# Optimization experiments

Measured on AMD Instinct MI355X. Metric: run time of the kernel, lower is better.

The kernel has to match this reference:

```python
import jax, jax.numpy as jnp
import numpy as np

N = 100000
H = 512
NUM_HEADS = 8
G = 512  # number of graphs (segments)


def seg_softmax(s, batch, num_segments):
    # numerically stable segment softmax (PyG-style, +1e-16 in denom)
    m = jax.ops.segment_max(s, batch, num_segments=num_segments)
    e = jnp.exp(s - m[batch])
    d = jax.ops.segment_sum(e, batch, num_segments=num_segments)
    return e / (d[batch] + 1e-16)


def setup_inputs() -> dict:
    key = jax.random.key(0)
    ks = jax.random.split(key, 12)
    s = 0.02
    x = jax.random.normal(ks[0], (N, H), dtype=jnp.float32)
    batch = jnp.sort(jax.random.randint(ks[1], (N,), 0, G)).astype(jnp.int64)
    # GlobalAttention.gate_nn: Linear(H, H//2) -> ReLU -> Linear(H//2, 1)
    ga_g_w1 = jax.random.normal(ks[2], (H, H // 2), dtype=jnp.float32) * s
    ga_g_b1 = jnp.zeros((H // 2,), dtype=jnp.float32)
    ga_g_w2 = jax.random.normal(ks[3], (H // 2, 1), dtype=jnp.float32) * s
    ga_g_b2 = jnp.zeros((1,), dtype=jnp.float32)
    # GlobalAttention.nn: Linear(H, H) -> ReLU
    ga_n_w = jax.random.normal(ks[4], (H, H), dtype=jnp.float32) * s
    ga_n_b = jnp.zeros((H,), dtype=jnp.float32)
    # outer gate_nn: Linear(H, H) -> ReLU -> (Dropout: identity in eval) -> Linear(H, NUM_HEADS)
    g_w1 = jax.random.normal(ks[5], (H, H), dtype=jnp.float32) * s
    g_b1 = jnp.zeros((H,), dtype=jnp.float32)
    g_w2 = jax.random.normal(ks[6], (H, NUM_HEADS), dtype=jnp.float32) * s
    g_b2 = jnp.zeros((NUM_HEADS,), dtype=jnp.float32)
    return dict(x=x, batch=batch,
                ga_g_w1=ga_g_w1, ga_g_b1=ga_g_b1, ga_g_w2=ga_g_w2, ga_g_b2=ga_g_b2,
                ga_n_w=ga_n_w, ga_n_b=ga_n_b,
                g_w1=g_w1, g_b1=g_b1, g_w2=g_w2, g_b2=g_b2)


def reference(x, batch, ga_g_w1, ga_g_b1, ga_g_w2, ga_g_b2, ga_n_w, ga_n_b,
              g_w1, g_b1, g_w2, g_b2):
    # --- GlobalAttention pooling ---
    h = jax.nn.relu(x @ ga_g_w1 + ga_g_b1)          # (N, H//2)
    gate = (h @ ga_g_w2 + ga_g_b2)[:, 0]            # (N,)
    gate = seg_softmax(gate, batch, G)              # segment softmax per graph
    xt = jax.nn.relu(x @ ga_n_w + ga_n_b)           # (N, H)
    graph_embedding = jax.ops.segment_sum(gate[:, None] * xt, batch,
                                          num_segments=G)  # (G, H)
    # --- interpretable attention weights ---
    g = jax.nn.relu(x @ g_w1 + g_b1)                # (N, H); dropout = identity (eval)
    scores = (g @ g_w2 + g_b2).mean(axis=-1)        # (N,) mean over heads
    attention = seg_softmax(scores, batch, G)       # (N,)
    return graph_embedding, attention
```

## Files before the change

kernel.cpp:

```cpp
#include <hip/hip_runtime.h>

#define NN 100000
#define HH 512
#define GG 512
#define NPACK 1280
#define NSTRIP 40
#define SB 32768
#define SB16 16384
#define XTROWS (NN + 128)

typedef unsigned short u16;
typedef unsigned int u32;
typedef __bf16 bf16x8 __attribute__((ext_vector_type(8)));
typedef unsigned short u16x8 __attribute__((ext_vector_type(8)));
typedef float f32x4 __attribute__((ext_vector_type(4)));
typedef __attribute__((address_space(1))) void gvoid_t;
typedef __attribute__((address_space(3))) void lvoid_t;

__device__ __forceinline__ u16 f2bf(float f) {
    unsigned u = __float_as_uint(f);
    unsigned r = u + 0x7FFFu + ((u >> 16) & 1u);
    return (u16)(r >> 16);
}
__device__ __forceinline__ float bf2f(u16 b) {
    return __uint_as_float(((unsigned)b) << 16);
}

__global__ __launch_bounds__(256)
void k_prep(const float* __restrict__ gw1, const float* __restrict__ gb1,
            const float* __restrict__ gw2v,
            const float* __restrict__ nw, const float* __restrict__ nbias,
            const float* __restrict__ aw1, const float* __restrict__ ab1,
            const float* __restrict__ aw2, const int* __restrict__ batch,
            u16* __restrict__ WT, float2* __restrict__ bwv,
            int* __restrict__ starts) {
    __shared__ u16 lt[64][80];
    const int b = blockIdx.x, tid = threadIdx.x;
    if (b < 160) {
        const int bn = b >> 3, bk = b & 7;
        const int N0 = bn * 64, K0 = bk * 64;
        const float* src; int LD, nb0;
        if (N0 < 256)      { src = gw1; LD = 256; nb0 = N0; }
        else if (N0 < 768) { src = nw;  LD = 512; nb0 = N0 - 256; }
        else               { src = aw1; LD = 512; nb0 = N0 - 768; }
        const int kr = tid >> 2, q = tid & 3;
        const float* sp = src + (size_t)(K0 + kr) * LD + nb0 + q * 16;
#pragma unroll
        for (int jj = 0; jj < 4; ++jj) {
            float4 f = *(const float4*)(sp + jj * 4);
            lt[q * 16 + jj * 4 + 0][kr] = f2bf(f.x);
            lt[q * 16 + jj * 4 + 1][kr] = f2bf(f.y);
            lt[q * 16 + jj * 4 + 2][kr] = f2bf(f.z);
            lt[q * 16 + jj * 4 + 3][kr] = f2bf(f.w);
        }
        __syncthreads();
        const int nlcl = tid >> 2, c2 = tid & 3;
        const int n = N0 + nlcl;
        const int s = n >> 4, nl = n & 15;
#pragma unroll
        for (int cc = 0; cc < 2; ++cc) {
            int c = c2 * 2 + cc;
            int ckb = (K0 >> 3) + c;
            size_t byte = (size_t)s * SB16 + nl * 1024 + ((size_t)(ckb ^ nl) << 4);
            *(u16x8*)((char*)WT + byte) = *(const u16x8*)(&lt[nlcl][c * 8]);
        }
    } else {
        for (int n = tid; n < NPACK; n += 256) {
            float bi, wv;
            if (n < 256)      { bi = gb1[n];        wv = gw2v[n]; }
            else if (n < 768) { bi = nbias[n - 256]; wv = 0.f; }
            else {
                bi = ab1[n - 768];
                float s = 0.f;
                for (int h = 0; h < 8; ++h) s += aw2[(n - 768) * 8 + h];
                wv = s * 0.125f;
            }
            bwv[n] = make_float2(bi, wv);
        }
        for (int g = tid; g <= GG; g += 256) {
            if (g == GG) { starts[GG] = NN; continue; }
            int lo = 0, hi = NN;
            while (lo < hi) { int mid = (lo + hi) >> 1; if (batch[mid] < g) lo = mid + 1; else hi = mid; }
            starts[g] = lo;
        }
    }
}

__global__ __launch_bounds__(256, 2)
void k_gemm(const float* __restrict__ X, const u16* __restrict__ B,
            const float2* __restrict__ bwv,
            const float* __restrict__ gb2, const float* __restrict__ ab2,
            u16* __restrict__ xt, float* __restrict__ gs, float* __restrict__ as_) {
    __shared__ __align__(16) char ldsB[2 * SB];
    __shared__ __align__(8) float2 bwv_lds[NPACK];

    const int tid = threadIdx.x;
    const int lane = tid & 63;
    const int w = tid >> 6;
    const int m0 = blockIdx.x * 128;
    const int l16 = lane & 15, kq = lane >> 4;

#define STAGE(s, bsel) do {                                                          \
    const char* _src = (const char*)B + (size_t)(s) * SB + tid * 16;                 \
    char* _dst = ldsB + (bsel) * SB + tid * 16;                                      \
    _Pragma("unroll")                                                                \
    for (int _t = 0; _t < 8; ++_t)                                                   \
        __builtin_amdgcn_global_load_lds((gvoid_t*)(_src + _t * 4096),               \
                                         (lvoid_t*)(_dst + _t * 4096), 16, 0, 0);    \
} while (0)

    STAGE(0, 0);

    for (int t = tid; t < NPACK; t += 256) bwv_lds[t] = bwv[t];

    float b2 = gb2[0];
    float bb = 0.f;
#pragma unroll
    for (int h = 0; h < 8; ++h) bb += ab2[h];
    bb *= 0.125f;

    bf16x8 a_reg[2][16];
#pragma unroll
    for (int i = 0; i < 2; ++i) {
        int row = m0 + w * 32 + i * 16 + l16;
        if (row >= NN) row = NN - 1;
        const float* xp = X + (size_t)row * 512 + kq * 8;
#pragma unroll
        for (int kt = 0; kt < 16; ++kt) {
            float4 f0 = *(const float4*)(xp + kt * 32);
            float4 f1 = *(const float4*)(xp + kt * 32 + 4);
            u16x8 u;
            u[0] = f2bf(f0.x); u[1] = f2bf(f0.y); u[2] = f2bf(f0.z); u[3] = f2bf(f0.w);
            u[4] = f2bf(f1.x); u[5] = f2bf(f1.y); u[6] = f2bf(f1.z); u[7] = f2bf(f1.w);
            a_reg[i][kt] = __builtin_bit_cast(bf16x8, u);
        }
    }

    float s_[2][4];
#pragma unroll
    for (int i = 0; i < 2; ++i)
#pragma unroll
        for (int r = 0; r < 4; ++r) s_[i][r] = 0.f;

    __syncthreads();

    for (int nt = 0; nt < NSTRIP; ++nt) {
        const int cur = nt & 1;

        if (nt >= 8 && nt <= 24) asm volatile("s_waitcnt vmcnt(8)" ::: "memory");
        else                     asm volatile("s_waitcnt vmcnt(0)" ::: "memory");
        __builtin_amdgcn_s_barrier();
        __builtin_amdgcn_sched_barrier(0);

        if (nt + 1 < NSTRIP) STAGE(nt + 1, cur ^ 1);

        f32x4 acc[2][2];
#pragma unroll
        for (int i = 0; i < 2; ++i) { acc[i][0] = {0.f,0.f,0.f,0.f}; acc[i][1] = {0.f,0.f,0.f,0.f}; }

        const char* bbase = ldsB + cur * SB + l16 * 1024;
        __builtin_amdgcn_s_setprio(1);
#pragma unroll
        for (int kt = 0; kt < 16; ++kt) {
            int off = ((kt * 4 + kq) ^ l16) << 4;
            bf16x8 b0 = *(const bf16x8*)(bbase + off);
            bf16x8 b1 = *(const bf16x8*)(bbase + 16384 + off);
#pragma unroll
            for (int i = 0; i < 2; ++i) {
                acc[i][0] = __builtin_amdgcn_mfma_f32_16x16x32_bf16(a_reg[i][kt], b0, acc[i][0], 0, 0, 0);
                acc[i][1] = __builtin_amdgcn_mfma_f32_16x16x32_bf16(a_reg[i][kt], b1, acc[i][1], 0, 0, 0);
            }
        }
        __builtin_amdgcn_s_setprio(0);

        float2 bw0 = bwv_lds[nt * 32 + l16];
        float2 bw1 = bwv_lds[nt * 32 + 16 + l16];
        if (nt >= 8 && nt < 24) {
            const int sx = nt - 8;
#pragma unroll
            for (int i = 0; i < 2; ++i)
#pragma unroll
                for (int r = 0; r < 4; ++r) {
                    int rg = m0 + w * 32 + i * 16 + kq * 4 + r;
                    ushort2 st;
                    st.x = f2bf(fmaxf(acc[i][0][r] + bw0.x, 0.f));
                    st.y = f2bf(fmaxf(acc[i][1][r] + bw1.x, 0.f));
                    *(ushort2*)(xt + (size_t)rg * 512 + sx * 32 + l16 * 2) = st;
                }
        } else {
#pragma unroll
            for (int i = 0; i < 2; ++i)
#pragma unroll
                for (int r = 0; r < 4; ++r)
                    s_[i][r] += fmaxf(acc[i][0][r] + bw0.x, 0.f) * bw0.y
                              + fmaxf(acc[i][1][r] + bw1.x, 0.f) * bw1.y;
            if (nt == 7) {
#pragma unroll
                for (int i = 0; i < 2; ++i)
#pragma unroll
                    for (int r = 0; r < 4; ++r) {
                        float pg = s_[i][r];
                        pg += __shfl_xor(pg, 1); pg += __shfl_xor(pg, 2);
                        pg += __shfl_xor(pg, 4); pg += __shfl_xor(pg, 8);
                        int rg = m0 + w * 32 + i * 16 + kq * 4 + r;
                        if (l16 == 0 && rg < NN) gs[rg] = pg + b2;
                        s_[i][r] = 0.f;
                    }
            }
        }
    }
#undef STAGE

#pragma unroll
    for (int i = 0; i < 2; ++i)
#pragma unroll
        for (int r = 0; r < 4; ++r) {
            float pa = s_[i][r];
            pa += __shfl_xor(pa, 1); pa += __shfl_xor(pa, 2);
            pa += __shfl_xor(pa, 4); pa += __shfl_xor(pa, 8);
            int rg = m0 + w * 32 + i * 16 + kq * 4 + r;
            if (l16 == 0 && rg < NN) as_[rg] = pa + bb;
        }
}

__global__ __launch_bounds__(256)
void k_post(const float* __restrict__ gs, const float* __restrict__ as_,
            const u16* __restrict__ xt, const int* __restrict__ starts,
            float* __restrict__ out_emb, float* __restrict__ out_att) {
    const int g = blockIdx.x;
    const int s0 = starts[g], s1 = starts[g + 1];
    const int tid = threadIdx.x, lane = tid & 63, w = tid >> 6;
    __shared__ float red[8];
    __shared__ float gbuf[1024];

    float lmg = -3.0e38f, lma = -3.0e38f;
    for (int i = s0 + tid; i < s1; i += 256) {
        lmg = fmaxf(lmg, gs[i]); lma = fmaxf(lma, as_[i]);
    }
    for (int o = 32; o; o >>= 1) {
        lmg = fmaxf(lmg, __shfl_xor(lmg, o));
        lma = fmaxf(lma, __shfl_xor(lma, o));
    }
    if (lane == 0) { red[w] = lmg; red[4 + w] = lma; }
    __syncthreads();
    float Mg = fmaxf(fmaxf(red[0], red[1]), fmaxf(red[2], red[3]));
    float Ma = fmaxf(fmaxf(red[4], red[5]), fmaxf(red[6], red[7]));
    __syncthreads();
    float sgv = 0.f, sav = 0.f;
    for (int i = s0 + tid; i < s1; i += 256) {
        sgv += expf(gs[i] - Mg); sav += expf(as_[i] - Ma);
    }
    for (int o = 32; o; o >>= 1) { sgv += __shfl_xor(sgv, o); sav += __shfl_xor(sav, o); }
    if (lane == 0) { red[w] = sgv; red[4 + w] = sav; }
    __syncthreads();
    const float Dg = red[0] + red[1] + red[2] + red[3] + 1e-16f;
    const float Da = red[4] + red[5] + red[6] + red[7] + 1e-16f;

    const int c2 = tid;
    const int col0 = (c2 >> 4) * 32 + (c2 & 15);
    float a0 = 0.f, a1 = 0.f;
    for (int nb = s0; nb < s1; nb += 1024) {
        const int ce = min(s1, nb + 1024);
        __syncthreads();
        for (int i = nb + tid; i < ce; i += 256) {
            gbuf[i - nb] = expf(gs[i] - Mg) / Dg;
            out_att[i]   = expf(as_[i] - Ma) / Da;
        }
        __syncthreads();
        const int cl = ce - nb;
        int j = 0;
        for (; j + 4 <= cl; j += 4) {
            const size_t n = (size_t)(nb + j);
            ushort2 u0 = ((const ushort2*)(xt + (n + 0) * 512))[c2];
            ushort2 u1 = ((const ushort2*)(xt + (n + 1) * 512))[c2];
            ushort2 u2 = ((const ushort2*)(xt + (n + 2) * 512))[c2];
            ushort2 u3 = ((const ushort2*)(xt + (n + 3) * 512))[c2];
            float g0 = gbuf[j], g1 = gbuf[j + 1], g2 = gbuf[j + 2], g3 = gbuf[j + 3];
            a0 += g0 * bf2f(u0.x); a1 += g0 * bf2f(u0.y);
            a0 += g1 * bf2f(u1.x); a1 += g1 * bf2f(u1.y);
            a0 += g2 * bf2f(u2.x); a1 += g2 * bf2f(u2.y);
            a0 += g3 * bf2f(u3.x); a1 += g3 * bf2f(u3.y);
        }
        for (; j < cl; ++j) {
            ushort2 u = ((const ushort2*)(xt + (size_t)(nb + j) * 512))[c2];
            float gj = gbuf[j];
            a0 += gj * bf2f(u.x); a1 += gj * bf2f(u.y);
        }
    }
    out_emb[g * 512 + col0] = a0;
    out_emb[g * 512 + col0 + 16] = a1;
}

extern "C" void kernel_launch(void* const* d_in, const int* in_sizes, int n_in,
                              void* d_out, int out_size, void* d_ws, size_t ws_size,
                              hipStream_t stream) {
    const float* x       = (const float*)d_in[0];
    const int*   batch   = (const int*)d_in[1];
    const float* ga_g_w1 = (const float*)d_in[2];
    const float* ga_g_b1 = (const float*)d_in[3];
    const float* ga_g_w2 = (const float*)d_in[4];
    const float* ga_g_b2 = (const float*)d_in[5];
    const float* ga_n_w  = (const float*)d_in[6];
    const float* ga_n_b  = (const float*)d_in[7];
    const float* g_w1    = (const float*)d_in[8];
    const float* g_b1    = (const float*)d_in[9];
    const float* g_w2    = (const float*)d_in[10];
    const float* g_b2    = (const float*)d_in[11];

    float* out_emb = (float*)d_out;
    float* out_att = out_emb + GG * HH;

    char* p = (char*)d_ws;
    size_t off = 0;
    auto alloc = [&](size_t bytes) -> char* {
        char* q = p + off;
        off += (bytes + 255) & ~(size_t)255;
        return q;
    };
    u16*    xt    = (u16*)   alloc((size_t)XTROWS * HH * 2);
    u16*    WT    = (u16*)   alloc((size_t)NPACK * 512 * 2);
    float2* bwv   = (float2*)alloc(NPACK * 8);
    float*  gs    = (float*) alloc((size_t)NN * 4);
    float*  as_   = (float*) alloc((size_t)NN * 4);
    int*    starts= (int*)   alloc((GG + 1) * 4);

    k_prep<<<161, 256, 0, stream>>>(ga_g_w1, ga_g_b1, ga_g_w2, ga_n_w, ga_n_b,
                                    g_w1, g_b1, g_w2, batch, WT, bwv, starts);
    k_gemm<<<782, 256, 0, stream>>>(x, WT, bwv, ga_g_b2, g_b2, xt, gs, as_);
    k_post<<<GG, 256, 0, stream>>>(gs, as_, xt, starts, out_emb, out_att);
}
```

Before: 487.0 us.

## Read packed weights directly from global memory instead of LDS double-buffering

The GEMM kernel stops staging weight strips into LDS through async global-to-LDS loads with double buffering and barriers. Each wave now loads its B fragments straight from a plain row-major packed weight layout in global memory, relying on L1/L2 caching, and reads the bias/weight pairs from global memory too. The prep kernel writes that unswizzled layout. The post kernel's segment-sum loop is also unrolled from 4 to 8 rows. This removes LDS traffic and barriers and frees LDS for occupancy, but the four waves now issue redundant global loads and lose explicit prefetch overlap.

```diff
diff --git a/kernel.cpp b/kernel.cpp
--- a/kernel.cpp
+++ b/kernel.cpp
@@ -5,8 +5,6 @@
 #define GG 512
 #define NPACK 1280
 #define NSTRIP 40
-#define SB 32768
-#define SB16 16384
 #define XTROWS (NN + 128)
 
 typedef unsigned short u16;
@@ -14,8 +12,6 @@
 typedef __bf16 bf16x8 __attribute__((ext_vector_type(8)));
 typedef unsigned short u16x8 __attribute__((ext_vector_type(8)));
 typedef float f32x4 __attribute__((ext_vector_type(4)));
-typedef __attribute__((address_space(1))) void gvoid_t;
-typedef __attribute__((address_space(3))) void lvoid_t;
 
 __device__ __forceinline__ u16 f2bf(float f) {
     unsigned u = __float_as_uint(f);
@@ -56,12 +52,10 @@
         __syncthreads();
         const int nlcl = tid >> 2, c2 = tid & 3;
         const int n = N0 + nlcl;
-        const int s = n >> 4, nl = n & 15;
 #pragma unroll
         for (int cc = 0; cc < 2; ++cc) {
             int c = c2 * 2 + cc;
-            int ckb = (K0 >> 3) + c;
-            size_t byte = (size_t)s * SB16 + nl * 1024 + ((size_t)(ckb ^ nl) << 4);
+            size_t byte = (size_t)n * 1024 + (size_t)(K0 / 8 + c) * 16;
             *(u16x8*)((char*)WT + byte) = *(const u16x8*)(&lt[nlcl][c * 8]);
         }
     } else {
@@ -91,27 +85,11 @@
             const float2* __restrict__ bwv,
             const float* __restrict__ gb2, const float* __restrict__ ab2,
             u16* __restrict__ xt, float* __restrict__ gs, float* __restrict__ as_) {
-    __shared__ __align__(16) char ldsB[2 * SB];
-    __shared__ __align__(8) float2 bwv_lds[NPACK];
-
     const int tid = threadIdx.x;
     const int lane = tid & 63;
     const int w = tid >> 6;
     const int m0 = blockIdx.x * 128;
     const int l16 = lane & 15, kq = lane >> 4;
-
-#define STAGE(s, bsel) do {                                                          \
-    const char* _src = (const char*)B + (size_t)(s) * SB + tid * 16;                 \
-    char* _dst = ldsB + (bsel) * SB + tid * 16;                                      \
-    _Pragma("unroll")                                                                \
-    for (int _t = 0; _t < 8; ++_t)                                                   \
-        __builtin_amdgcn_global_load_lds((gvoid_t*)(_src + _t * 4096),               \
-                                         (lvoid_t*)(_dst + _t * 4096), 16, 0, 0);    \
-} while (0)
-
-    STAGE(0, 0);
-
-    for (int t = tid; t < NPACK; t += 256) bwv_lds[t] = bwv[t];
 
     float b2 = gb2[0];
     float bb = 0.f;
@@ -142,39 +120,29 @@
 #pragma unroll
         for (int r = 0; r < 4; ++r) s_[i][r] = 0.f;
 
-    __syncthreads();
+    const u16* bp = B + (size_t)l16 * 512 + kq * 8;
 
     for (int nt = 0; nt < NSTRIP; ++nt) {
-        const int cur = nt & 1;
-
-        if (nt >= 8 && nt <= 24) asm volatile("s_waitcnt vmcnt(8)" ::: "memory");
-        else                     asm volatile("s_waitcnt vmcnt(0)" ::: "memory");
-        __builtin_amdgcn_s_barrier();
-        __builtin_amdgcn_sched_barrier(0);
-
-        if (nt + 1 < NSTRIP) STAGE(nt + 1, cur ^ 1);
+        const u16* bp0 = bp + (size_t)nt * 32 * 512;
+        const u16* bp1 = bp0 + 16 * 512;
 
         f32x4 acc[2][2];
 #pragma unroll
         for (int i = 0; i < 2; ++i) { acc[i][0] = {0.f,0.f,0.f,0.f}; acc[i][1] = {0.f,0.f,0.f,0.f}; }
 
-        const char* bbase = ldsB + cur * SB + l16 * 1024;
-        __builtin_amdgcn_s_setprio(1);
 #pragma unroll
         for (int kt = 0; kt < 16; ++kt) {
-            int off = ((kt * 4 + kq) ^ l16) << 4;
-            bf16x8 b0 = *(const bf16x8*)(bbase + off);
-            bf16x8 b1 = *(const bf16x8*)(bbase + 16384 + off);
+            bf16x8 b0 = *(const bf16x8*)(bp0 + kt * 32);
+            bf16x8 b1 = *(const bf16x8*)(bp1 + kt * 32);
 #pragma unroll
             for (int i = 0; i < 2; ++i) {
                 acc[i][0] = __builtin_amdgcn_mfma_f32_16x16x32_bf16(a_reg[i][kt], b0, acc[i][0], 0, 0, 0);
                 acc[i][1] = __builtin_amdgcn_mfma_f32_16x16x32_bf16(a_reg[i][kt], b1, acc[i][1], 0, 0, 0);
             }
         }
-        __builtin_amdgcn_s_setprio(0);
-
-        float2 bw0 = bwv_lds[nt * 32 + l16];
-        float2 bw1 = bwv_lds[nt * 32 + 16 + l16];
+
+        float2 bw0 = bwv[nt * 32 + l16];
+        float2 bw1 = bwv[nt * 32 + 16 + l16];
         if (nt >= 8 && nt < 24) {
             const int sx = nt - 8;
 #pragma unroll
@@ -209,7 +177,6 @@
             }
         }
     }
-#undef STAGE
 
 #pragma unroll
     for (int i = 0; i < 2; ++i)
@@ -269,17 +236,26 @@
         __syncthreads();
         const int cl = ce - nb;
         int j = 0;
-        for (; j + 4 <= cl; j += 4) {
+        for (; j + 8 <= cl; j += 8) {
             const size_t n = (size_t)(nb + j);
             ushort2 u0 = ((const ushort2*)(xt + (n + 0) * 512))[c2];
             ushort2 u1 = ((const ushort2*)(xt + (n + 1) * 512))[c2];
             ushort2 u2 = ((const ushort2*)(xt + (n + 2) * 512))[c2];
             ushort2 u3 = ((const ushort2*)(xt + (n + 3) * 512))[c2];
-            float g0 = gbuf[j], g1 = gbuf[j + 1], g2 = gbuf[j + 2], g3 = gbuf[j + 3];
+            ushort2 u4 = ((const ushort2*)(xt + (n + 4) * 512))[c2];
+            ushort2 u5 = ((const ushort2*)(xt + (n + 5) * 512))[c2];
+            ushort2 u6 = ((const ushort2*)(xt + (n + 6) * 512))[c2];
+            ushort2 u7 = ((const ushort2*)(xt + (n + 7) * 512))[c2];
+            float g0 = gbuf[j],     g1 = gbuf[j + 1], g2 = gbuf[j + 2], g3 = gbuf[j + 3];
+            float g4 = gbuf[j + 4], g5 = gbuf[j + 5], g6 = gbuf[j + 6], g7 = gbuf[j + 7];
             a0 += g0 * bf2f(u0.x); a1 += g0 * bf2f(u0.y);
             a0 += g1 * bf2f(u1.x); a1 += g1 * bf2f(u1.y);
             a0 += g2 * bf2f(u2.x); a1 += g2 * bf2f(u2.y);
             a0 += g3 * bf2f(u3.x); a1 += g3 * bf2f(u3.y);
+            a0 += g4 * bf2f(u4.x); a1 += g4 * bf2f(u4.y);
+            a0 += g5 * bf2f(u5.x); a1 += g5 * bf2f(u5.y);
+            a0 += g6 * bf2f(u6.x); a1 += g6 * bf2f(u6.y);
+            a0 += g7 * bf2f(u7.x); a1 += g7 * bf2f(u7.y);
         }
         for (; j < cl; ++j) {
             ushort2 u = ((const ushort2*)(xt + (size_t)(nb + j) * 512))[c2];
```

Measured after the change: 924.0 us. 89.7% more time.
